# Kernel optimization log

Measured on AMD Instinct MI355X. Metric: run time of the kernel, lower is better.

## Reference

```python
import jax, jax.numpy as jnp
import numpy as np

B, S = 64, 2048
ENC_DIM, DEC_DIM, ATT_DIM = 1024, 1024, 512


def setup_inputs() -> dict:
    key = jax.random.key(0)
    k1, k2, k3, k4, k5, k6 = jax.random.split(key, 6)
    # parameters follow torch kaiming_uniform_(a=sqrt(5)) -> U(-1/sqrt(fan_in), 1/sqrt(fan_in)) scale approx
    def uni(k, shape, fan_in):
        b = 1.0 / np.sqrt(fan_in)
        return jax.random.uniform(k, shape, jnp.float32, -b, b)
    return {
        "decoder_hidden": jax.random.normal(k1, (B, DEC_DIM), jnp.float32),
        "encoder_outputs": jax.random.normal(k2, (B, S, ENC_DIM), jnp.float32),
        "mask": jax.random.randint(k3, (B, S), 0, 2) > 0,
        "W_enc": uni(k4, (ATT_DIM, ENC_DIM), ENC_DIM),   # encoder_projection.weight
        "W_dec": uni(k5, (ATT_DIM, DEC_DIM), DEC_DIM),   # decoder_projection.weight
        "W_energy": uni(k6, (1, ATT_DIM), ATT_DIM),      # energy_projection.weight
    }


def reference(decoder_hidden, encoder_outputs, mask, W_enc, W_dec, W_energy):
    # decoder_features: [B, 1, A]
    dec_feat = (decoder_hidden @ W_dec.T)[:, None, :]
    # encoder_features: [B, S, A]
    enc_feat = jnp.einsum("bse,ae->bsa", encoder_outputs, W_enc)
    energy = jnp.tanh(enc_feat + dec_feat)                     # [B, S, A]
    scores = jnp.einsum("bsa,a->bs", energy, W_energy[0])      # [B, S]
    scores = jnp.where(mask, jnp.finfo(scores.dtype).min, scores)
    attention_weights = jax.nn.softmax(scores, axis=-1)        # [B, S]
    context = jnp.einsum("bs,bse->be", attention_weights, encoder_outputs)
    return context, attention_weights
```

## Files before the change

kernel.cpp:

```cpp
#include <hip/hip_runtime.h>
#include <stdint.h>

#define B_ 64
#define S_ 2048
#define E_ 1024
#define D_ 1024
#define A_ 512
#define M_ (B_*S_)

typedef __attribute__((ext_vector_type(8))) short short8;
typedef __attribute__((ext_vector_type(4))) float floatx4;

typedef __attribute__((address_space(3))) void       lds_void_t;
typedef const __attribute__((address_space(1))) void gbl_void_t;

__device__ __forceinline__ unsigned short f2bf(float f) {
    union { float f; uint32_t u; } v; v.f = f;
    uint32_t u = v.u;
    return (unsigned short)((u + 0x7FFF + ((u >> 16) & 1)) >> 16);
}

__global__ void k_convert_wenc(const float* __restrict__ wenc,
                               unsigned short* __restrict__ out) {
    int i = blockIdx.x * 256 + threadIdx.x;
    float4 v = ((const float4*)wenc)[i];
    ushort4 o;
    o.x = f2bf(v.x); o.y = f2bf(v.y); o.z = f2bf(v.z); o.w = f2bf(v.w);
    ((ushort4*)out)[i] = o;
}

__global__ void k_dec_feat(const float* __restrict__ dh,
                           const float* __restrict__ wdec,
                           float* __restrict__ df) {
    __shared__ float h[D_];
    int b = blockIdx.x, t = threadIdx.x;
    for (int i = t; i < D_/4; i += 256)
        ((float4*)h)[i] = ((const float4*)(dh + (size_t)b * D_))[i];
    __syncthreads();
    #pragma unroll
    for (int rep = 0; rep < 2; ++rep) {
        int a = t + rep * 256;
        const float4* wr = (const float4*)(wdec + (size_t)a * D_);
        float acc = 0.f;
        for (int k4 = 0; k4 < D_/4; ++k4) {
            float4 w = wr[k4];
            float4 x = ((float4*)h)[k4];
            acc += w.x*x.x + w.y*x.y + w.z*x.z + w.w*x.w;
        }
        df[b * A_ + a] = acc;
    }
}

#define BM 64
#define BK 32

__global__ __launch_bounds__(256, 2) void k_scores(
    const float* __restrict__ enc,
    const unsigned short* __restrict__ wenc,
    const float* __restrict__ df,
    const float* __restrict__ wE,
    float* __restrict__ scores)
{
    __shared__ unsigned short As[BM * BK];
    __shared__ unsigned short Bs[A_ * BK];
    __shared__ float ps[4][BM];

    const int tid  = threadIdx.x;
    const int wave = tid >> 6;
    const int lane = tid & 63;
    const int m0   = blockIdx.x * BM;
    const int b    = m0 >> 11;

    floatx4 acc[4][8];
    #pragma unroll
    for (int i = 0; i < 4; ++i)
        #pragma unroll
        for (int j = 0; j < 8; ++j) acc[i][j] = (floatx4)0.f;

    const int m_a = tid >> 2;
    const int k_a = (tid & 3) * 8;
    const float* aptr = enc + (size_t)(m0 + m_a) * E_ + k_a;

    const int n0w   = wave * 128;
    const int row16 = lane >> 4;
    const int col   = lane & 15;

    for (int kt = 0; kt < E_ / BK; ++kt) {
        if (kt) __syncthreads();
        float4 a0 = *(const float4*)(aptr + kt * BK);
        float4 a1 = *(const float4*)(aptr + kt * BK + 4);
        short8 apk;
        apk[0] = (short)f2bf(a0.x); apk[1] = (short)f2bf(a0.y);
        apk[2] = (short)f2bf(a0.z); apk[3] = (short)f2bf(a0.w);
        apk[4] = (short)f2bf(a1.x); apk[5] = (short)f2bf(a1.y);
        apk[6] = (short)f2bf(a1.z); apk[7] = (short)f2bf(a1.w);
        *(short8*)(&As[m_a * BK + k_a]) = apk;
        #pragma unroll
        for (int r = 0; r < 8; ++r) {
            int idx = r * 256 + tid;
            int n   = idx >> 2;
            int kq  = idx & 3;
            const unsigned short* g = wenc + (size_t)n * E_ + kt * BK + kq * 8;
            unsigned short* l = &Bs[(size_t)(r * 256 + wave * 64) * 8];
            __builtin_amdgcn_global_load_lds((gbl_void_t*)g, (lds_void_t*)l, 16, 0, 0);
        }
        __syncthreads();
        short8 af[4];
        #pragma unroll
        for (int mt = 0; mt < 4; ++mt)
            af[mt] = *(const short8*)(&As[(mt * 16 + col) * BK + row16 * 8]);
        short8 bfr[8];
        #pragma unroll
        for (int nt = 0; nt < 8; ++nt)
            bfr[nt] = *(const short8*)(&Bs[(n0w + nt * 16 + col) * BK + row16 * 8]);
        #pragma unroll
        for (int mt = 0; mt < 4; ++mt)
            #pragma unroll
            for (int nt = 0; nt < 8; ++nt)
                acc[mt][nt] = __builtin_amdgcn_mfma_f32_16x16x32_bf16(
                    af[mt], bfr[nt], acc[mt][nt], 0, 0, 0);
    }

    float part[4][4];
    #pragma unroll
    for (int mt = 0; mt < 4; ++mt)
        #pragma unroll
        for (int r = 0; r < 4; ++r) part[mt][r] = 0.f;

    #pragma unroll
    for (int nt = 0; nt < 8; ++nt) {
        int n   = n0w + nt * 16 + col;
        float d = df[b * A_ + n];
        float w = wE[n];
        #pragma unroll
        for (int mt = 0; mt < 4; ++mt)
            #pragma unroll
            for (int r = 0; r < 4; ++r) {
                float x  = acc[mt][nt][r] + d;
                float ex = __expf(2.f * x);
                float th = 1.f - 2.f / (ex + 1.f);
                part[mt][r] += w * th;
            }
    }
    #pragma unroll
    for (int mt = 0; mt < 4; ++mt)
        #pragma unroll
        for (int r = 0; r < 4; ++r) {
            float v = part[mt][r];
            v += __shfl_xor(v, 1);
            v += __shfl_xor(v, 2);
            v += __shfl_xor(v, 4);
            v += __shfl_xor(v, 8);
            part[mt][r] = v;
        }
    if (col == 0) {
        #pragma unroll
        for (int mt = 0; mt < 4; ++mt)
            #pragma unroll
            for (int r = 0; r < 4; ++r)
                ps[wave][mt * 16 + row16 * 4 + r] = part[mt][r];
    }
    __syncthreads();
    if (tid < BM)
        scores[m0 + tid] = ps[0][tid] + ps[1][tid] + ps[2][tid] + ps[3][tid];
}

__global__ void k_softmax(const float* __restrict__ scores,
                          const int* __restrict__ mask,
                          float* __restrict__ weights) {
    __shared__ float red[8];
    int b = blockIdx.x, t = threadIdx.x;
    float v[8];
    #pragma unroll
    for (int i = 0; i < 8; ++i) {
        int s = t + i * 256;
        float x = scores[b * S_ + s];
        v[i] = mask[b * S_ + s] ? -3.402823466e38f : x;
    }
    float mx = v[0];
    #pragma unroll
    for (int i = 1; i < 8; ++i) mx = fmaxf(mx, v[i]);
    #pragma unroll
    for (int o = 32; o; o >>= 1) mx = fmaxf(mx, __shfl_xor(mx, o));
    if ((t & 63) == 0) red[t >> 6] = mx;
    __syncthreads();
    mx = fmaxf(fmaxf(red[0], red[1]), fmaxf(red[2], red[3]));

    float e[8], sum = 0.f;
    #pragma unroll
    for (int i = 0; i < 8; ++i) { e[i] = __expf(v[i] - mx); sum += e[i]; }
    #pragma unroll
    for (int o = 32; o; o >>= 1) sum += __shfl_xor(sum, o);
    if ((t & 63) == 0) red[4 + (t >> 6)] = sum;
    __syncthreads();
    sum = red[4] + red[5] + red[6] + red[7];
    float inv = 1.f / sum;
    #pragma unroll
    for (int i = 0; i < 8; ++i)
        weights[b * S_ + t + i * 256] = e[i] * inv;
}

__global__ void k_context(const float* __restrict__ enc,
                          const float* __restrict__ weights,
                          float* __restrict__ ctx) {
    int b  = blockIdx.x >> 4;
    int sc = blockIdx.x & 15;
    int t  = threadIdx.x;
    const float* ep = enc + (size_t)b * S_ * E_ + (size_t)sc * 128 * E_ + t * 4;
    const float* wp = weights + b * S_ + sc * 128;
    float4 acc = {0.f, 0.f, 0.f, 0.f};
    for (int s = 0; s < 128; ++s) {
        float w  = wp[s];
        float4 x = *(const float4*)(ep + (size_t)s * E_);
        acc.x += w * x.x; acc.y += w * x.y; acc.z += w * x.z; acc.w += w * x.w;
    }
    float* o = ctx + (size_t)b * E_ + t * 4;
    atomicAdd(o + 0, acc.x); atomicAdd(o + 1, acc.y);
    atomicAdd(o + 2, acc.z); atomicAdd(o + 3, acc.w);
}

extern "C" void kernel_launch(void* const* d_in, const int* in_sizes, int n_in,
                              void* d_out, int out_size, void* d_ws, size_t ws_size,
                              hipStream_t stream) {
    const float* dh   = (const float*)d_in[0];
    const float* enc  = (const float*)d_in[1];
    const int*   mask = (const int*)  d_in[2];
    const float* wenc = (const float*)d_in[3];
    const float* wdec = (const float*)d_in[4];
    const float* wE   = (const float*)d_in[5];

    float* out     = (float*)d_out;
    float* ctx     = out;
    float* weights = out + B_ * E_;

    unsigned short* wenc_bf = (unsigned short*)d_ws;
    float* df     = (float*)((char*)d_ws + (size_t)A_ * E_ * 2);
    float* scores = df + B_ * A_;

    hipMemsetAsync(ctx, 0, (size_t)B_ * E_ * sizeof(float), stream);
    k_convert_wenc<<<512, 256, 0, stream>>>(wenc, wenc_bf);
    k_dec_feat<<<B_, 256, 0, stream>>>(dh, wdec, df);
    k_scores<<<M_ / BM, 256, 0, stream>>>(enc, wenc_bf, df, wE, scores);
    k_softmax<<<B_, 256, 0, stream>>>(scores, mask, weights);
    k_context<<<B_ * 16, 256, 0, stream>>>(enc, weights, ctx);
}
```

Baseline: 992.2 us.

## Pre-swizzle W_enc layout, pad LDS, parallelize dec_feat, batch context loads

The W_enc bf16 conversion now writes a k-chunk-major, swizzled layout. The scores kernel can then stream each k-tile contiguously into LDS and read B fragments without bank conflicts. The A tile row stride is padded to 40 to avoid LDS bank conflicts, and the async weight loads are issued before the A conversion for overlap. dec_feat is split across 8x more blocks with a 4-way k split and shuffle reduction. The context kernel batches 8 row loads per iteration over larger chunks, halving the number of atomics.

After: 902.9 us. -9.0%, faster.

```diff
diff --git a/kernel.cpp b/kernel.cpp
--- a/kernel.cpp
+++ b/kernel.cpp
@@ -21,48 +21,63 @@
 }
 
 __global__ void k_convert_wenc(const float* __restrict__ wenc,
-                               unsigned short* __restrict__ out) {
-    int i = blockIdx.x * 256 + threadIdx.x;
-    float4 v = ((const float4*)wenc)[i];
-    ushort4 o;
-    o.x = f2bf(v.x); o.y = f2bf(v.y); o.z = f2bf(v.z); o.w = f2bf(v.w);
-    ((ushort4*)out)[i] = o;
+                               unsigned short* __restrict__ wencS) {
+    int slot = blockIdx.x * 256 + threadIdx.x;
+    int kt = slot >> 11;
+    int kq = (slot >> 9) & 3;
+    int n  = slot & 511;
+    const float4* src = (const float4*)(wenc + (size_t)n * E_ + kt * 32 + kq * 8);
+    float4 a = src[0], b = src[1];
+    short8 o;
+    o[0] = (short)f2bf(a.x); o[1] = (short)f2bf(a.y);
+    o[2] = (short)f2bf(a.z); o[3] = (short)f2bf(a.w);
+    o[4] = (short)f2bf(b.x); o[5] = (short)f2bf(b.y);
+    o[6] = (short)f2bf(b.z); o[7] = (short)f2bf(b.w);
+    *(short8*)(wencS + (size_t)slot * 8) = o;
 }
 
 __global__ void k_dec_feat(const float* __restrict__ dh,
                            const float* __restrict__ wdec,
                            float* __restrict__ df) {
-    __shared__ float h[D_];
-    int b = blockIdx.x, t = threadIdx.x;
-    for (int i = t; i < D_/4; i += 256)
-        ((float4*)h)[i] = ((const float4*)(dh + (size_t)b * D_))[i];
-    __syncthreads();
-    #pragma unroll
-    for (int rep = 0; rep < 2; ++rep) {
-        int a = t + rep * 256;
-        const float4* wr = (const float4*)(wdec + (size_t)a * D_);
-        float acc = 0.f;
-        for (int k4 = 0; k4 < D_/4; ++k4) {
-            float4 w = wr[k4];
-            float4 x = ((float4*)h)[k4];
-            acc += w.x*x.x + w.y*x.y + w.z*x.z + w.w*x.w;
-        }
-        df[b * A_ + a] = acc;
-    }
+    __shared__ float h[1056];
+    int b  = blockIdx.x >> 3;
+    int a0 = (blockIdx.x & 7) * 64;
+    int t  = threadIdx.x;
+    {
+        float4 v = ((const float4*)(dh + (size_t)b * D_))[t];
+        int e0 = t * 4;
+        *(float4*)(h + (e0 >> 8) * 264 + (e0 & 255)) = v;
+    }
+    __syncthreads();
+    int a  = a0 + (t >> 2);
+    int kq = t & 3;
+    const float4* wr = (const float4*)(wdec + (size_t)a * D_ + kq * 256);
+    const float4* hh = (const float4*)(h + kq * 264);
+    float acc = 0.f;
+    #pragma unroll 8
+    for (int k4 = 0; k4 < 64; ++k4) {
+        float4 w = wr[k4];
+        float4 x = hh[k4];
+        acc += w.x*x.x + w.y*x.y + w.z*x.z + w.w*x.w;
+    }
+    acc += __shfl_xor(acc, 1);
+    acc += __shfl_xor(acc, 2);
+    if ((t & 3) == 0) df[b * A_ + a] = acc;
 }
 
 #define BM 64
 #define BK 32
+#define AROW 40
 
 __global__ __launch_bounds__(256, 2) void k_scores(
     const float* __restrict__ enc,
-    const unsigned short* __restrict__ wenc,
+    const unsigned short* __restrict__ wencS,
     const float* __restrict__ df,
     const float* __restrict__ wE,
     float* __restrict__ scores)
 {
-    __shared__ unsigned short As[BM * BK];
-    __shared__ unsigned short Bs[A_ * BK];
+    __shared__ unsigned short As[BM * AROW];
+    __shared__ unsigned short Bs[4 * 512 * 8];
     __shared__ float ps[4][BM];
 
     const int tid  = threadIdx.x;
@@ -78,8 +93,8 @@
         for (int j = 0; j < 8; ++j) acc[i][j] = (floatx4)0.f;
 
     const int m_a = tid >> 2;
-    const int k_a = (tid & 3) * 8;
-    const float* aptr = enc + (size_t)(m0 + m_a) * E_ + k_a;
+    const int j_a = tid & 3;
+    const float* aptr = enc + (size_t)(m0 + m_a) * E_ + j_a * 8;
 
     const int n0w   = wave * 128;
     const int row16 = lane >> 4;
@@ -89,30 +104,28 @@
         if (kt) __syncthreads();
         float4 a0 = *(const float4*)(aptr + kt * BK);
         float4 a1 = *(const float4*)(aptr + kt * BK + 4);
+        #pragma unroll
+        for (int r = 0; r < 8; ++r) {
+            int s = r * 256 + tid;
+            const unsigned short* g = wencS + ((size_t)kt * 2048 + s) * 8;
+            unsigned short* l = &Bs[(size_t)(r * 256 + wave * 64) * 8];
+            __builtin_amdgcn_global_load_lds((gbl_void_t*)g, (lds_void_t*)l, 16, 0, 0);
+        }
         short8 apk;
         apk[0] = (short)f2bf(a0.x); apk[1] = (short)f2bf(a0.y);
         apk[2] = (short)f2bf(a0.z); apk[3] = (short)f2bf(a0.w);
         apk[4] = (short)f2bf(a1.x); apk[5] = (short)f2bf(a1.y);
         apk[6] = (short)f2bf(a1.z); apk[7] = (short)f2bf(a1.w);
-        *(short8*)(&As[m_a * BK + k_a]) = apk;
-        #pragma unroll
-        for (int r = 0; r < 8; ++r) {
-            int idx = r * 256 + tid;
-            int n   = idx >> 2;
-            int kq  = idx & 3;
-            const unsigned short* g = wenc + (size_t)n * E_ + kt * BK + kq * 8;
-            unsigned short* l = &Bs[(size_t)(r * 256 + wave * 64) * 8];
-            __builtin_amdgcn_global_load_lds((gbl_void_t*)g, (lds_void_t*)l, 16, 0, 0);
-        }
+        *(short8*)(&As[m_a * AROW + j_a * 8]) = apk;
         __syncthreads();
         short8 af[4];
         #pragma unroll
         for (int mt = 0; mt < 4; ++mt)
-            af[mt] = *(const short8*)(&As[(mt * 16 + col) * BK + row16 * 8]);
+            af[mt] = *(const short8*)(&As[(mt * 16 + col) * AROW + row16 * 8]);
         short8 bfr[8];
         #pragma unroll
         for (int nt = 0; nt < 8; ++nt)
-            bfr[nt] = *(const short8*)(&Bs[(n0w + nt * 16 + col) * BK + row16 * 8]);
+            bfr[nt] = *(const short8*)(&Bs[(size_t)(row16 * 512 + n0w + nt * 16 + col) * 8]);
         #pragma unroll
         for (int mt = 0; mt < 4; ++mt)
             #pragma unroll
@@ -203,16 +216,23 @@
 __global__ void k_context(const float* __restrict__ enc,
                           const float* __restrict__ weights,
                           float* __restrict__ ctx) {
-    int b  = blockIdx.x >> 4;
-    int sc = blockIdx.x & 15;
+    int b  = blockIdx.x >> 3;
+    int sc = blockIdx.x & 7;
     int t  = threadIdx.x;
-    const float* ep = enc + (size_t)b * S_ * E_ + (size_t)sc * 128 * E_ + t * 4;
-    const float* wp = weights + b * S_ + sc * 128;
+    const float4* ep = (const float4*)(enc + (size_t)b * S_ * E_ + (size_t)sc * 256 * E_) + t;
+    const float*  wp = weights + b * S_ + sc * 256;
     float4 acc = {0.f, 0.f, 0.f, 0.f};
-    for (int s = 0; s < 128; ++s) {
-        float w  = wp[s];
-        float4 x = *(const float4*)(ep + (size_t)s * E_);
-        acc.x += w * x.x; acc.y += w * x.y; acc.z += w * x.z; acc.w += w * x.w;
+    for (int s0 = 0; s0 < 256; s0 += 8) {
+        float4 x[8];
+        #pragma unroll
+        for (int i = 0; i < 8; ++i)
+            x[i] = ep[(size_t)(s0 + i) * (E_ / 4)];
+        #pragma unroll
+        for (int i = 0; i < 8; ++i) {
+            float w = wp[s0 + i];
+            acc.x += w * x[i].x; acc.y += w * x[i].y;
+            acc.z += w * x[i].z; acc.w += w * x[i].w;
+        }
     }
     float* o = ctx + (size_t)b * E_ + t * 4;
     atomicAdd(o + 0, acc.x); atomicAdd(o + 1, acc.y);
@@ -233,14 +253,14 @@
     float* ctx     = out;
     float* weights = out + B_ * E_;
 
-    unsigned short* wenc_bf = (unsigned short*)d_ws;
+    unsigned short* wencS = (unsigned short*)d_ws;
     float* df     = (float*)((char*)d_ws + (size_t)A_ * E_ * 2);
     float* scores = df + B_ * A_;
 
     hipMemsetAsync(ctx, 0, (size_t)B_ * E_ * sizeof(float), stream);
-    k_convert_wenc<<<512, 256, 0, stream>>>(wenc, wenc_bf);
-    k_dec_feat<<<B_, 256, 0, stream>>>(dh, wdec, df);
-    k_scores<<<M_ / BM, 256, 0, stream>>>(enc, wenc_bf, df, wE, scores);
+    k_convert_wenc<<<256, 256, 0, stream>>>(wenc, wencS);
+    k_dec_feat<<<B_ * 8, 256, 0, stream>>>(dh, wdec, df);
+    k_scores<<<M_ / BM, 256, 0, stream>>>(enc, wencS, df, wE, scores);
     k_softmax<<<B_, 256, 0, stream>>>(scores, mask, weights);
-    k_context<<<B_ * 16, 256, 0, stream>>>(enc, weights, ctx);
-}
+    k_context<<<B_ * 8, 256, 0, stream>>>(enc, weights, ctx);
+}
```
